# Optimization experiments

Hardware: AMD Instinct MI355X
Metric: run time of the kernel (lower is better)

Reference implementation:

```python
import jax, jax.numpy as jnp
import numpy as np

N_NODES = 90  # hard-coded per-graph node count in the original module
HIDDEN = 128


def setup_inputs() -> dict:
    key = jax.random.key(0)
    ks = jax.random.split(key, 12)
    B = 8192
    adj = jax.random.uniform(ks[0], (B, N_NODES, N_NODES), dtype=jnp.float32)
    s_in = 1.0 / np.sqrt(N_NODES)
    s_h = 1.0 / np.sqrt(HIDDEN)
    return {
        "adj": adj,
        "W_mlp0": jax.random.normal(ks[1], (N_NODES, HIDDEN), jnp.float32) * s_in,
        "b_mlp0": jax.random.normal(ks[2], (HIDDEN,), jnp.float32) * s_in,
        "W_mlp1": jax.random.normal(ks[3], (HIDDEN, HIDDEN), jnp.float32) * s_h,
        "b_mlp1": jax.random.normal(ks[4], (HIDDEN,), jnp.float32) * s_h,
        "W_mlp2": jax.random.normal(ks[5], (HIDDEN, HIDDEN), jnp.float32) * s_h,
        "b_mlp2": jax.random.normal(ks[6], (HIDDEN,), jnp.float32) * s_h,
        "W_res1": jax.random.normal(ks[7], (HIDDEN, HIDDEN), jnp.float32) * s_h,
        "b_res1": jax.random.normal(ks[8], (HIDDEN,), jnp.float32) * s_h,
        "W_res2": jax.random.normal(ks[9], (HIDDEN, HIDDEN), jnp.float32) * s_h,
        "b_res2": jax.random.normal(ks[10], (HIDDEN,), jnp.float32) * s_h,
    }


def reference(adj, W_mlp0, b_mlp0, W_mlp1, b_mlp1, W_mlp2, b_mlp2,
              W_res1, b_res1, W_res2, b_res2):
    B = adj.shape[0]
    # raw node features: identity per graph (torch.eye(90) concatenated)
    raw_x = jnp.broadcast_to(jnp.eye(N_NODES, dtype=adj.dtype), (B, N_NODES, N_NODES))

    def gconv(x, W, b):
        # block-diagonal Adj_block @ x == batched per-graph matmul, then linear
        return jnp.einsum('bij,bjk->bik', adj, x) @ W + b

    # encoding == 1 branch, layers = 3
    h0 = gconv(raw_x, W_mlp0, b_mlp0)                    # mlps[0](raw_x, A)
    r1 = h0 @ W_res1 + b_res1                            # res[1](h0)
    x = jax.nn.relu(gconv(h0, W_mlp1, b_mlp1)) + r1      # layer 1
    Y = jax.nn.relu(gconv(x, W_mlp2, b_mlp2) + (r1 @ W_res2 + b_res2))  # final

    # decoder: per-graph inner-product, concatenated along node axis
    Z = jnp.einsum('bik,bjk->bij', Y, Y)                 # [B, 90, 90]
    return Z.reshape(B * N_NODES, N_NODES)
```

## Files before the change

### kernel.cpp

```cpp
#include <hip/hip_runtime.h>


#define NN 90
#define HH 128
#define NT 256

typedef _Float16 half8 __attribute__((ext_vector_type(8)));
typedef _Float16 half2v __attribute__((ext_vector_type(2)));
typedef float floatx16 __attribute__((ext_vector_type(16)));
typedef unsigned int uint4v __attribute__((ext_vector_type(4)));

#define AST 104
#define AST8 13
#define ASTU 52
#define SR 136
#define SR8 17

#define MFMA(a, b, c) __builtin_amdgcn_mfma_f32_32x32x16_f16((a), (b), (c), 0, 0, 0)

__global__ void prep_weights(const float* __restrict__ W0,
                             const float* __restrict__ Wr1,
                             const float* __restrict__ W1,
                             const float* __restrict__ W2,
                             const float* __restrict__ Wr2,
                             const float* __restrict__ b2,
                             const float* __restrict__ br1,
                             const float* __restrict__ br2,
                             _Float16* __restrict__ ws)
{
    const int idx = blockIdx.x * blockDim.x + threadIdx.x;
    if (idx < 12288) {
        const int nn = idx / 96, k = idx - nn * 96;
        if (k != 90)
            ws[idx] = (k < NN) ? (_Float16)W0[k * HH + nn] : (_Float16)0.f;
    } else if (idx < 61440) {
        const int j = idx - 12288;
        const int m = j >> 14;
        const int r = j & 16383;
        const int nn = r >> 7, k = r & 127;
        const float* src = (m == 0) ? Wr1 : (m == 1) ? W1 : W2;
        ws[idx] = (_Float16)src[k * HH + nn];
    } else if (idx < 77824) {
        const int j = idx - 61440;
        const int nn = j >> 7, k = j & 127;
        float s = 0.f;
        for (int q = 0; q < HH; q++) s += Wr1[k * HH + q] * Wr2[q * HH + nn];
        ws[idx] = (_Float16)s;
    } else if (idx < 77952) {
        const int nn = idx - 77824;
        float s = b2[nn] + br2[nn];
        for (int q = 0; q < HH; q++) s += br1[q] * Wr2[q * HH + nn];
        ws[nn * 96 + 90] = (_Float16)s;
    }
}

__global__ __launch_bounds__(NT, 2) void graphcnn_mfma(
    const float* __restrict__ adj,
    const _Float16* __restrict__ wts,
    const float* __restrict__ b0, const float* __restrict__ b1,
    const float* __restrict__ br1,
    float* __restrict__ out)
{
    __shared__ __align__(16) unsigned char smem[72192];
    _Float16* adjH = (_Float16*)smem;
    _Float16* B1   = (_Float16*)(smem + 19968);
    _Float16* B2   = (_Float16*)(smem + 46080);

    const int t    = threadIdx.x;
    const int wv   = t >> 6;
    const int lane = t & 63;
    const int p    = lane & 31;
    const int h    = lane >> 5;
    const int n    = wv * 32 + p;

    const _Float16* W0T  = wts;
    const _Float16* Wr1T = wts + 12288;
    const _Float16* W1T  = wts + 28672;
    const _Float16* W2T  = wts + 45056;
    const _Float16* WcT  = wts + 61440;

    {
        const float* Ag = adj + (size_t)blockIdx.x * (NN * NN);
        unsigned* aH = (unsigned*)adjH;
        #pragma unroll
        for (int it = 0; it < 18; it++) {
            const int i = t + it * NT;
            const int r = i / 48, cc = i - r * 48;
            unsigned val = 0u;
            if (r < NN && cc < 45) {
                const float2 v = *(const float2*)(Ag + r * NN + cc * 2);
                const half2v hv = { (_Float16)v.x, (_Float16)v.y };
                val = __builtin_bit_cast(unsigned, hv);
            }
            aH[r * ASTU + cc] = val;
        }
    }

    auto writeR = [&](_Float16* buf, const floatx16& A0, const floatx16& A1,
                      const floatx16& A2) {
        #pragma unroll
        for (int mt = 0; mt < 3; mt++) {
            const floatx16& A = (mt == 0) ? A0 : (mt == 1) ? A1 : A2;
            #pragma unroll
            for (int r = 0; r < 16; r++) {
                const int node = mt * 32 + (r & 3) + 8 * (r >> 2) + 4 * h;
                buf[node * SR + n] = (_Float16)A[r];
            }
        }
    };

    uint4v frg[6];
    auto buildFrags = [&](const floatx16& A0, const floatx16& A1, const floatx16& A2) {
        #pragma unroll
        for (int mt = 0; mt < 3; mt++) {
            const floatx16& A = (mt == 0) ? A0 : (mt == 1) ? A1 : A2;
            #pragma unroll
            for (int s01 = 0; s01 < 2; s01++) {
                const int s = 8 * s01;
                const half2v x0 = { (_Float16)A[s + 0], (_Float16)A[s + 1] };
                const half2v x1 = { (_Float16)A[s + 2], (_Float16)A[s + 3] };
                const half2v y0 = { (_Float16)A[s + 4], (_Float16)A[s + 5] };
                const half2v y1 = { (_Float16)A[s + 6], (_Float16)A[s + 7] };
                const unsigned X0 = __builtin_bit_cast(unsigned, x0);
                const unsigned X1 = __builtin_bit_cast(unsigned, x1);
                const unsigned Y0 = __builtin_bit_cast(unsigned, y0);
                const unsigned Y1 = __builtin_bit_cast(unsigned, y1);
                const unsigned R0 = __shfl_xor(h ? X0 : Y0, 32, 64);
                const unsigned R1 = __shfl_xor(h ? X1 : Y1, 32, 64);
                uint4v f;
                f[0] = h ? R0 : X0;
                f[1] = h ? R1 : X1;
                f[2] = h ? Y0 : R0;
                f[3] = h ? Y1 : R1;
                frg[mt * 2 + s01] = f;
            }
        }
    };

    __syncthreads();

    floatx16 acc0, acc1, acc2;

    {
        half8 bw[6];
        #pragma unroll
        for (int kt = 0; kt < 6; kt++) bw[kt] = ((const half8*)W0T)[n * 12 + kt * 2 + h];
        const float bias = b0[n];
        #pragma unroll
        for (int r = 0; r < 16; r++) { acc0[r] = bias; acc1[r] = bias; acc2[r] = bias; }
        #pragma unroll
        for (int kt = 0; kt < 6; kt++) {
            const half8 a0 = ((const half8*)adjH)[(0 * 32 + p) * AST8 + kt * 2 + h];
            const half8 a1 = ((const half8*)adjH)[(1 * 32 + p) * AST8 + kt * 2 + h];
            const half8 a2 = ((const half8*)adjH)[(2 * 32 + p) * AST8 + kt * 2 + h];
            acc0 = MFMA(a0, bw[kt], acc0);
            acc1 = MFMA(a1, bw[kt], acc1);
            acc2 = MFMA(a2, bw[kt], acc2);
        }
        writeR(B2, acc0, acc1, acc2);
        buildFrags(acc0, acc1, acc2);
    }

    {
        #pragma unroll
        for (int r = 0; r < 16; r++) { acc0[r] = 0.f; acc1[r] = 0.f; acc2[r] = 0.f; }
        #pragma unroll
        for (int kt = 0; kt < 6; kt++) {
            const half8 bfk = __builtin_bit_cast(half8, frg[kt]);
            const half8 a0 = ((const half8*)adjH)[(0 * 32 + p) * AST8 + kt * 2 + h];
            const half8 a1 = ((const half8*)adjH)[(1 * 32 + p) * AST8 + kt * 2 + h];
            const half8 a2 = ((const half8*)adjH)[(2 * 32 + p) * AST8 + kt * 2 + h];
            acc0 = MFMA(a0, bfk, acc0);
            acc1 = MFMA(a1, bfk, acc1);
            acc2 = MFMA(a2, bfk, acc2);
        }
        writeR(B1, acc0, acc1, acc2);
    }
    __syncthreads();

    floatx16 r1a, r1b, r1c;
    {
        half8 bw[8];
        #pragma unroll
        for (int kt = 0; kt < 8; kt++) bw[kt] = ((const half8*)Wr1T)[n * 16 + kt * 2 + h];
        const float bias = br1[n];
        #pragma unroll
        for (int r = 0; r < 16; r++) { r1a[r] = bias; r1b[r] = bias; r1c[r] = bias; }
        #pragma unroll
        for (int kt = 0; kt < 8; kt++) {
            const half8 a0 = ((const half8*)B2)[(0 * 32 + p) * SR8 + kt * 2 + h];
            const half8 a1 = ((const half8*)B2)[(1 * 32 + p) * SR8 + kt * 2 + h];
            const half8 a2 = ((const half8*)B2)[(2 * 32 + p) * SR8 + kt * 2 + h];
            r1a = MFMA(a0, bw[kt], r1a);
            r1b = MFMA(a1, bw[kt], r1b);
            r1c = MFMA(a2, bw[kt], r1c);
        }
    }

    {
        half8 bw[8];
        #pragma unroll
        for (int kt = 0; kt < 8; kt++) bw[kt] = ((const half8*)W1T)[n * 16 + kt * 2 + h];
        const float bias = b1[n];
        #pragma unroll
        for (int r = 0; r < 16; r++) { acc0[r] = bias; acc1[r] = bias; acc2[r] = bias; }
        #pragma unroll
        for (int kt = 0; kt < 8; kt++) {
            const half8 a0 = ((const half8*)B1)[(0 * 32 + p) * SR8 + kt * 2 + h];
            const half8 a1 = ((const half8*)B1)[(1 * 32 + p) * SR8 + kt * 2 + h];
            const half8 a2 = ((const half8*)B1)[(2 * 32 + p) * SR8 + kt * 2 + h];
            acc0 = MFMA(a0, bw[kt], acc0);
            acc1 = MFMA(a1, bw[kt], acc1);
            acc2 = MFMA(a2, bw[kt], acc2);
        }
        #pragma unroll
        for (int r = 0; r < 16; r++) {
            acc0[r] = fmaxf(acc0[r], 0.f) + r1a[r];
            acc1[r] = fmaxf(acc1[r], 0.f) + r1b[r];
            acc2[r] = fmaxf(acc2[r], 0.f) + r1c[r];
        }
        buildFrags(acc0, acc1, acc2);
    }
    __syncthreads();

    {
        #pragma unroll
        for (int r = 0; r < 16; r++) { acc0[r] = 0.f; acc1[r] = 0.f; acc2[r] = 0.f; }
        #pragma unroll
        for (int kt = 0; kt < 6; kt++) {
            const half8 bfk = __builtin_bit_cast(half8, frg[kt]);
            const half8 a0 = ((const half8*)adjH)[(0 * 32 + p) * AST8 + kt * 2 + h];
            const half8 a1 = ((const half8*)adjH)[(1 * 32 + p) * AST8 + kt * 2 + h];
            const half8 a2 = ((const half8*)adjH)[(2 * 32 + p) * AST8 + kt * 2 + h];
            acc0 = MFMA(a0, bfk, acc0);
            acc1 = MFMA(a1, bfk, acc1);
            acc2 = MFMA(a2, bfk, acc2);
        }
        writeR(B1, acc0, acc1, acc2);
    }
    __syncthreads();

    {
        half8 bw[8], bg[8];
        #pragma unroll
        for (int kt = 0; kt < 8; kt++) {
            bw[kt] = ((const half8*)W2T)[n * 16 + kt * 2 + h];
            bg[kt] = ((const half8*)WcT)[n * 16 + kt * 2 + h];
        }
        const float bias = (float)W0T[n * 96 + 90];
        #pragma unroll
        for (int r = 0; r < 16; r++) { acc0[r] = bias; acc1[r] = bias; acc2[r] = bias; }
        #pragma unroll
        for (int kt = 0; kt < 8; kt++) {
            const half8 a0 = ((const half8*)B1)[(0 * 32 + p) * SR8 + kt * 2 + h];
            const half8 a1 = ((const half8*)B1)[(1 * 32 + p) * SR8 + kt * 2 + h];
            const half8 a2 = ((const half8*)B1)[(2 * 32 + p) * SR8 + kt * 2 + h];
            acc0 = MFMA(a0, bw[kt], acc0);
            acc1 = MFMA(a1, bw[kt], acc1);
            acc2 = MFMA(a2, bw[kt], acc2);
        }
        #pragma unroll
        for (int kt = 0; kt < 8; kt++) {
            const half8 a0 = ((const half8*)B2)[(0 * 32 + p) * SR8 + kt * 2 + h];
            const half8 a1 = ((const half8*)B2)[(1 * 32 + p) * SR8 + kt * 2 + h];
            const half8 a2 = ((const half8*)B2)[(2 * 32 + p) * SR8 + kt * 2 + h];
            acc0 = MFMA(a0, bg[kt], acc0);
            acc1 = MFMA(a1, bg[kt], acc1);
            acc2 = MFMA(a2, bg[kt], acc2);
        }
    }
    __syncthreads();
    {
        _Float16* YR = B2;
        #pragma unroll
        for (int mt = 0; mt < 3; mt++) {
            const floatx16& A = (mt == 0) ? acc0 : (mt == 1) ? acc1 : acc2;
            #pragma unroll
            for (int r = 0; r < 16; r++) {
                const int node = mt * 32 + (r & 3) + 8 * (r >> 2) + 4 * h;
                YR[node * SR + n] = (_Float16)fmaxf(A[r], 0.f);
            }
        }
    }
    __syncthreads();

    {
        const _Float16* YR = B2;
        float* outb = out + (size_t)blockIdx.x * (NN * NN);
        auto ztile = [&](int mt, int nt) {
            floatx16 acc;
            #pragma unroll
            for (int r = 0; r < 16; r++) acc[r] = 0.f;
            #pragma unroll
            for (int kt = 0; kt < 8; kt++) {
                const half8 av = ((const half8*)YR)[(mt * 32 + p) * SR8 + kt * 2 + h];
                const half8 bv = ((const half8*)YR)[(nt * 32 + p) * SR8 + kt * 2 + h];
                acc = MFMA(av, bv, acc);
            }
            const int col = nt * 32 + p;
            if (col < NN) {
                #pragma unroll
                for (int r = 0; r < 16; r++) {
                    const int row = mt * 32 + (r & 3) + 8 * (r >> 2) + 4 * h;
                    if (row < NN) outb[row * NN + col] = acc[r];
                }
            }
        };
        if      (wv == 0) { ztile(0, 0); ztile(0, 1); ztile(0, 2); }
        else if (wv == 1) { ztile(1, 0); ztile(1, 1); }
        else if (wv == 2) { ztile(1, 2); ztile(2, 0); }
        else              { ztile(2, 1); ztile(2, 2); }
    }
}

extern "C" void kernel_launch(void* const* d_in, const int* in_sizes, int n_in,
                              void* d_out, int out_size, void* d_ws, size_t ws_size,
                              hipStream_t stream) {
    const float* adj = (const float*)d_in[0];
    const float* W0  = (const float*)d_in[1];
    const float* b0  = (const float*)d_in[2];
    const float* W1  = (const float*)d_in[3];
    const float* b1  = (const float*)d_in[4];
    const float* W2  = (const float*)d_in[5];
    const float* b2  = (const float*)d_in[6];
    const float* Wr1 = (const float*)d_in[7];
    const float* br1 = (const float*)d_in[8];
    const float* Wr2 = (const float*)d_in[9];
    const float* br2 = (const float*)d_in[10];
    float* out = (float*)d_out;
    _Float16* wts = (_Float16*)d_ws;

    prep_weights<<<77, 1024, 0, stream>>>(W0, Wr1, W1, W2, Wr2, b2, br1, br2, wts);

    const int B = in_sizes[0] / (NN * NN);
    graphcnn_mfma<<<B, NT, 0, stream>>>(adj, wts, b0, b1, br1, out);
}
```

Before: 749.0 us.

## Fold residual weights into adjacency-side products to drop B2 buffer and raise occupancy

Precomputes W0·Wr1 and (W0·Wr1)·Wr2 plus folded biases on the device, so r1 and its second residual term come straight from adj in K=96 matmuls. This replaces the K=128 products that read h0 from a second shared buffer. Removing that buffer cuts LDS per block from about 72KB to 46KB, and launch bounds rise to 3 blocks per CU. The cost is an extra prep kernel and the r1 residual being kept in fp16 registers, which adds rounding error, plus possible register pressure at the higher occupancy target.

```diff
diff --git a/kernel.cpp b/kernel.cpp
--- a/kernel.cpp
+++ b/kernel.cpp
@@ -18,53 +18,82 @@
 
 #define MFMA(a, b, c) __builtin_amdgcn_mfma_f32_32x32x16_f16((a), (b), (c), 0, 0, 0)
 
-__global__ void prep_weights(const float* __restrict__ W0,
-                             const float* __restrict__ Wr1,
-                             const float* __restrict__ W1,
-                             const float* __restrict__ W2,
-                             const float* __restrict__ Wr2,
-                             const float* __restrict__ b2,
-                             const float* __restrict__ br1,
-                             const float* __restrict__ br2,
-                             _Float16* __restrict__ ws)
+__global__ void prep_stage1(const float* __restrict__ W0,
+                            const float* __restrict__ Wr1,
+                            const float* __restrict__ b0,
+                            const float* __restrict__ br1,
+                            float* __restrict__ WdF,
+                            float* __restrict__ c1F)
+{
+    const int idx = blockIdx.x * blockDim.x + threadIdx.x;
+    if (idx < NN * HH) {
+        const int k = idx >> 7, nn = idx & 127;
+        float s = 0.f;
+        for (int q = 0; q < HH; q++) s += W0[k * HH + q] * Wr1[q * HH + nn];
+        WdF[idx] = s;
+    } else if (idx < NN * HH + HH) {
+        const int nn = idx - NN * HH;
+        float s = br1[nn];
+        for (int q = 0; q < HH; q++) s += b0[q] * Wr1[q * HH + nn];
+        c1F[nn] = s;
+    }
+}
+
+__global__ void prep_stage2(const float* __restrict__ W0,
+                            const float* __restrict__ W1,
+                            const float* __restrict__ W2,
+                            const float* __restrict__ Wr2,
+                            const float* __restrict__ b2,
+                            const float* __restrict__ br2,
+                            const float* __restrict__ WdF,
+                            const float* __restrict__ c1F,
+                            _Float16* __restrict__ ws)
 {
     const int idx = blockIdx.x * blockDim.x + threadIdx.x;
     if (idx < 12288) {
         const int nn = idx / 96, k = idx - nn * 96;
-        if (k != 90)
-            ws[idx] = (k < NN) ? (_Float16)W0[k * HH + nn] : (_Float16)0.f;
-    } else if (idx < 61440) {
+        ws[idx] = (k < NN) ? (_Float16)W0[k * HH + nn] : (_Float16)0.f;
+    } else if (idx < 24576) {
         const int j = idx - 12288;
-        const int m = j >> 14;
-        const int r = j & 16383;
-        const int nn = r >> 7, k = r & 127;
-        const float* src = (m == 0) ? Wr1 : (m == 1) ? W1 : W2;
-        ws[idx] = (_Float16)src[k * HH + nn];
-    } else if (idx < 77824) {
-        const int j = idx - 61440;
+        const int nn = j / 96, k = j - nn * 96;
+        _Float16 v = (_Float16)0.f;
+        if (k < NN)       v = (_Float16)WdF[k * HH + nn];
+        else if (k == NN) v = (_Float16)c1F[nn];
+        ws[idx] = v;
+    } else if (idx < 36864) {
+        const int j = idx - 24576;
+        const int nn = j / 96, k = j - nn * 96;
+        _Float16 v = (_Float16)0.f;
+        if (k < NN) {
+            float s = 0.f;
+            for (int q = 0; q < HH; q++) s += WdF[k * HH + q] * Wr2[q * HH + nn];
+            v = (_Float16)s;
+        } else if (k == NN) {
+            float s = b2[nn] + br2[nn];
+            for (int q = 0; q < HH; q++) s += c1F[q] * Wr2[q * HH + nn];
+            v = (_Float16)s;
+        }
+        ws[idx] = v;
+    } else if (idx < 53248) {
+        const int j = idx - 36864;
         const int nn = j >> 7, k = j & 127;
-        float s = 0.f;
-        for (int q = 0; q < HH; q++) s += Wr1[k * HH + q] * Wr2[q * HH + nn];
-        ws[idx] = (_Float16)s;
-    } else if (idx < 77952) {
-        const int nn = idx - 77824;
-        float s = b2[nn] + br2[nn];
-        for (int q = 0; q < HH; q++) s += br1[q] * Wr2[q * HH + nn];
-        ws[nn * 96 + 90] = (_Float16)s;
+        ws[idx] = (_Float16)W1[k * HH + nn];
+    } else if (idx < 69632) {
+        const int j = idx - 53248;
+        const int nn = j >> 7, k = j & 127;
+        ws[idx] = (_Float16)W2[k * HH + nn];
     }
 }
 
-__global__ __launch_bounds__(NT, 2) void graphcnn_mfma(
+__global__ __launch_bounds__(NT, 3) void graphcnn_mfma(
     const float* __restrict__ adj,
     const _Float16* __restrict__ wts,
     const float* __restrict__ b0, const float* __restrict__ b1,
-    const float* __restrict__ br1,
     float* __restrict__ out)
 {
-    __shared__ __align__(16) unsigned char smem[72192];
+    __shared__ __align__(16) unsigned char smem[46080];
     _Float16* adjH = (_Float16*)smem;
     _Float16* B1   = (_Float16*)(smem + 19968);
-    _Float16* B2   = (_Float16*)(smem + 46080);
 
     const int t    = threadIdx.x;
     const int wv   = t >> 6;
@@ -73,11 +102,11 @@
     const int h    = lane >> 5;
     const int n    = wv * 32 + p;
 
-    const _Float16* W0T  = wts;
-    const _Float16* Wr1T = wts + 12288;
-    const _Float16* W1T  = wts + 28672;
-    const _Float16* W2T  = wts + 45056;
-    const _Float16* WcT  = wts + 61440;
+    const _Float16* W0T = wts;
+    const _Float16* WdT = wts + 12288;
+    const _Float16* WeT = wts + 24576;
+    const _Float16* W1T = wts + 36864;
+    const _Float16* W2T = wts + 53248;
 
     {
         const float* Ag = adj + (size_t)blockIdx.x * (NN * NN);
@@ -157,7 +186,6 @@
             acc1 = MFMA(a1, bw[kt], acc1);
             acc2 = MFMA(a2, bw[kt], acc2);
         }
-        writeR(B2, acc0, acc1, acc2);
         buildFrags(acc0, acc1, acc2);
     }
 
@@ -176,26 +204,38 @@
         }
         writeR(B1, acc0, acc1, acc2);
     }
-    __syncthreads();
-
-    floatx16 r1a, r1b, r1c;
-    {
-        half8 bw[8];
-        #pragma unroll
-        for (int kt = 0; kt < 8; kt++) bw[kt] = ((const half8*)Wr1T)[n * 16 + kt * 2 + h];
-        const float bias = br1[n];
-        #pragma unroll
-        for (int r = 0; r < 16; r++) { r1a[r] = bias; r1b[r] = bias; r1c[r] = bias; }
-        #pragma unroll
-        for (int kt = 0; kt < 8; kt++) {
-            const half8 a0 = ((const half8*)B2)[(0 * 32 + p) * SR8 + kt * 2 + h];
-            const half8 a1 = ((const half8*)B2)[(1 * 32 + p) * SR8 + kt * 2 + h];
-            const half8 a2 = ((const half8*)B2)[(2 * 32 + p) * SR8 + kt * 2 + h];
-            r1a = MFMA(a0, bw[kt], r1a);
-            r1b = MFMA(a1, bw[kt], r1b);
-            r1c = MFMA(a2, bw[kt], r1c);
-        }
-    }
+
+    half8 r1p[6];
+    {
+        half8 bw[6];
+        #pragma unroll
+        for (int kt = 0; kt < 6; kt++) bw[kt] = ((const half8*)WdT)[n * 12 + kt * 2 + h];
+        const float bias = (float)WdT[n * 96 + 90];
+        floatx16 ra, rb, rc;
+        #pragma unroll
+        for (int r = 0; r < 16; r++) { ra[r] = bias; rb[r] = bias; rc[r] = bias; }
+        #pragma unroll
+        for (int kt = 0; kt < 6; kt++) {
+            const half8 a0 = ((const half8*)adjH)[(0 * 32 + p) * AST8 + kt * 2 + h];
+            const half8 a1 = ((const half8*)adjH)[(1 * 32 + p) * AST8 + kt * 2 + h];
+            const half8 a2 = ((const half8*)adjH)[(2 * 32 + p) * AST8 + kt * 2 + h];
+            ra = MFMA(a0, bw[kt], ra);
+            rb = MFMA(a1, bw[kt], rb);
+            rc = MFMA(a2, bw[kt], rc);
+        }
+        #pragma unroll
+        for (int mt = 0; mt < 3; mt++) {
+            const floatx16& A = (mt == 0) ? ra : (mt == 1) ? rb : rc;
+            #pragma unroll
+            for (int s01 = 0; s01 < 2; s01++) {
+                half8 v;
+                #pragma unroll
+                for (int j = 0; j < 8; j++) v[j] = (_Float16)A[8 * s01 + j];
+                r1p[mt * 2 + s01] = v;
+            }
+        }
+    }
+    __syncthreads();
 
     {
         half8 bw[8];
@@ -215,9 +255,9 @@
         }
         #pragma unroll
         for (int r = 0; r < 16; r++) {
-            acc0[r] = fmaxf(acc0[r], 0.f) + r1a[r];
-            acc1[r] = fmaxf(acc1[r], 0.f) + r1b[r];
-            acc2[r] = fmaxf(acc2[r], 0.f) + r1c[r];
+            acc0[r] = fmaxf(acc0[r], 0.f) + (float)r1p[0 * 2 + (r >> 3)][r & 7];
+            acc1[r] = fmaxf(acc1[r], 0.f) + (float)r1p[1 * 2 + (r >> 3)][r & 7];
+            acc2[r] = fmaxf(acc2[r], 0.f) + (float)r1p[2 * 2 + (r >> 3)][r & 7];
         }
         buildFrags(acc0, acc1, acc2);
     }
@@ -241,13 +281,10 @@
     __syncthreads();
 
     {
-        half8 bw[8], bg[8];
-        #pragma unroll
-        for (int kt = 0; kt < 8; kt++) {
-            bw[kt] = ((const half8*)W2T)[n * 16 + kt * 2 + h];
-            bg[kt] = ((const half8*)WcT)[n * 16 + kt * 2 + h];
-        }
-        const float bias = (float)W0T[n * 96 + 90];
+        half8 bw[8];
+        #pragma unroll
+        for (int kt = 0; kt < 8; kt++) bw[kt] = ((const half8*)W2T)[n * 16 + kt * 2 + h];
+        const float bias = (float)WeT[n * 96 + 90];
         #pragma unroll
         for (int r = 0; r < 16; r++) { acc0[r] = bias; acc1[r] = bias; acc2[r] = bias; }
         #pragma unroll
@@ -259,11 +296,14 @@
             acc1 = MFMA(a1, bw[kt], acc1);
             acc2 = MFMA(a2, bw[kt], acc2);
         }
-        #pragma unroll
-        for (int kt = 0; kt < 8; kt++) {
-            const half8 a0 = ((const half8*)B2)[(0 * 32 + p) * SR8 + kt * 2 + h];
-            const half8 a1 = ((const half8*)B2)[(1 * 32 + p) * SR8 + kt * 2 + h];
-            const half8 a2 = ((const half8*)B2)[(2 * 32 + p) * SR8 + kt * 2 + h];
+        half8 bg[6];
+        #pragma unroll
+        for (int kt = 0; kt < 6; kt++) bg[kt] = ((const half8*)WeT)[n * 12 + kt * 2 + h];
+        #pragma unroll
+        for (int kt = 0; kt < 6; kt++) {
+            const half8 a0 = ((const half8*)adjH)[(0 * 32 + p) * AST8 + kt * 2 + h];
+            const half8 a1 = ((const half8*)adjH)[(1 * 32 + p) * AST8 + kt * 2 + h];
+            const half8 a2 = ((const half8*)adjH)[(2 * 32 + p) * AST8 + kt * 2 + h];
             acc0 = MFMA(a0, bg[kt], acc0);
             acc1 = MFMA(a1, bg[kt], acc1);
             acc2 = MFMA(a2, bg[kt], acc2);
@@ -271,7 +311,7 @@
     }
     __syncthreads();
     {
-        _Float16* YR = B2;
+        _Float16* YR = B1;
         #pragma unroll
         for (int mt = 0; mt < 3; mt++) {
             const floatx16& A = (mt == 0) ? acc0 : (mt == 1) ? acc1 : acc2;
@@ -285,7 +325,7 @@
     __syncthreads();
 
     {
-        const _Float16* YR = B2;
+        const _Float16* YR = B1;
         float* outb = out + (size_t)blockIdx.x * (NN * NN);
         auto ztile = [&](int mt, int nt) {
             floatx16 acc;
@@ -330,8 +370,12 @@
     float* out = (float*)d_out;
     _Float16* wts = (_Float16*)d_ws;
 
-    prep_weights<<<77, 1024, 0, stream>>>(W0, Wr1, W1, W2, Wr2, b2, br1, br2, wts);
+    float* WdF = (float*)((char*)d_ws + 139264);
+    float* c1F = (float*)((char*)d_ws + 185344);
+
+    prep_stage1<<<12, 1024, 0, stream>>>(W0, Wr1, b0, br1, WdF, c1F);
+    prep_stage2<<<68, 1024, 0, stream>>>(W0, W1, W2, Wr2, b2, br2, WdF, c1F, wts);
 
     const int B = in_sizes[0] / (NN * NN);
-    graphcnn_mfma<<<B, NT, 0, stream>>>(adj, wts, b0, b1, br1, out);
+    graphcnn_mfma<<<B, NT, 0, stream>>>(adj, wts, b0, b1, out);
 }
```

Result: faster. 681.0 us (-9.1%).
